# Performance work log

Hardware: AMD Instinct MI355X
Metric: run time of the kernel (lower is better)

## Reference

```python
import jax, jax.numpy as jnp
import numpy as np

B, N, E, DIN, DOUT = 8, 4096, 160, 15, 15


def _mha(q, k, v, in_w, in_b, out_w, out_b, h):
    # torch.nn.MultiheadAttention math: packed in_proj, per-head scaled dot attn, out_proj.
    e = q.shape[-1]
    d = e // h
    scale = 1.0 / np.sqrt(d)

    def proj(x, w, b):
        y = x @ w.T + b
        return jnp.moveaxis(y.reshape(y.shape[:-1] + (h, d)), -2, -3)  # [..., h, L, d]

    qh = proj(q, in_w[:e], in_b[:e])
    kh = proj(k, in_w[e:2 * e], in_b[e:2 * e])
    vh = proj(v, in_w[2 * e:], in_b[2 * e:])
    a = jax.nn.softmax(jnp.einsum('...hld,...hmd->...hlm', qh, kh) * scale, axis=-1)
    o = jnp.einsum('...hlm,...hmd->...hld', a, vh)
    o = jnp.moveaxis(o, -3, -2).reshape(q.shape)
    return o @ out_w.T + out_b


def _attn_layer(seq, Wq, Wk, Wv, in_w, in_b, out_w, out_b, h):
    # AttentionLayer: extra Wq/Wk/Wv projections feeding the MHA
    return _mha(seq @ Wq, seq @ Wk, seq @ Wv, in_w, in_b, out_w, out_b, h)


def setup_inputs():
    key = jax.random.key(0)
    ks = jax.random.split(key, 20)
    s = 1.0 / np.sqrt(E)
    p = lambda i, shape: jax.random.normal(ks[i], shape, dtype=jnp.float32) * s
    return {
        'X_batch': jax.random.normal(ks[0], (B, N, E), dtype=jnp.float32),
        'in_idx': jax.random.randint(ks[1], (B, N, DIN), 0, N),
        'out_idx': jax.random.randint(ks[2], (B, N, DOUT), 0, N),
        'iWq': p(3, (E, E)), 'iWk': p(4, (E, E)), 'iWv': p(5, (E, E)),
        'i_in_w': p(6, (3 * E, E)), 'i_in_b': jnp.zeros(3 * E, jnp.float32),
        'i_out_w': p(7, (E, E)), 'i_out_b': jnp.zeros(E, jnp.float32),
        'oWq': p(8, (E, E)), 'oWk': p(9, (E, E)), 'oWv': p(10, (E, E)),
        'o_in_w': p(11, (3 * E, E)), 'o_in_b': jnp.zeros(3 * E, jnp.float32),
        'o_out_w': p(12, (E, E)), 'o_out_b': jnp.zeros(E, jnp.float32),
        'f_in_w': p(13, (3 * E, E)), 'f_in_b': jnp.zeros(3 * E, jnp.float32),
        'f_out_w': p(14, (E, E)), 'f_out_b': jnp.zeros(E, jnp.float32),
        'lin_w': p(15, (E, E)), 'lin_b': jnp.zeros(E, jnp.float32),
    }


def reference(X_batch, in_idx, out_idx,
              iWq, iWk, iWv, i_in_w, i_in_b, i_out_w, i_out_b,
              oWq, oWk, oWv, o_in_w, o_in_b, o_out_w, o_out_b,
              f_in_w, f_in_b, f_out_w, f_out_b, lin_w, lin_b):
    b_ix = jnp.arange(X_batch.shape[0])[:, None, None]
    self_f = X_batch[:, :, None, :]                                   # [B,N,1,E]
    seq_in = jnp.concatenate([self_f, X_batch[b_ix, in_idx]], axis=2)  # [B,N,1+DIN,E]
    seq_out = jnp.concatenate([self_f, X_batch[b_ix, out_idx]], axis=2)
    a_in = _attn_layer(seq_in, iWq, iWk, iWv, i_in_w, i_in_b, i_out_w, i_out_b, 5)
    a_out = _attn_layer(seq_out, oWq, oWk, oWv, o_in_w, o_in_b, o_out_w, o_out_b, 5)
    a = jnp.concatenate([a_in, a_out], axis=2)                         # [B,N,2+DIN+DOUT,E]
    f = _mha(a, a, a, f_in_w, f_in_b, f_out_w, f_out_b, 1)
    pooled = jnp.max(f, axis=2)                                        # max over sequence dim
    return jax.nn.elu(pooled @ lin_w.T + lin_b)
```

## Files before the change

### kernel.cpp

```cpp
#include <hip/hip_runtime.h>
#include <hip/hip_bf16.h>
#include <math.h>

#define NTH 256

typedef __bf16 bf16x8 __attribute__((ext_vector_type(8)));
typedef float  f32x4  __attribute__((ext_vector_type(4)));
typedef unsigned short ushort;
typedef ushort u16x8 __attribute__((ext_vector_type(8)));

__device__ __forceinline__ ushort f2bf(float x){
    union { float f; unsigned int u; } v; v.f = x;
    unsigned int r = v.u + 0x7fffu + ((v.u >> 16) & 1u);
    return (ushort)(r >> 16);
}
__device__ __forceinline__ float bf2f(ushort h){
    union { unsigned int u; float f; } v; v.u = ((unsigned int)h) << 16;
    return v.f;
}

__global__ void prep_combined_bf(const float* __restrict__ Wq, const float* __restrict__ Wk,
                                 const float* __restrict__ Wv, const float* __restrict__ in_w,
                                 ushort* __restrict__ dh)
{
    int o = blockIdx.x*NTH + threadIdx.x;
    if (o >= 76800) return;
    int c = o/160, j = o - c*160;
    const float* Wsel = (c<160) ? Wq : (c<320) ? Wk : Wv;
    const float* wrow = Wsel + j*160;
    const float* irow = in_w + c*160;
    float s = 0.f;
    for (int k=0;k<160;k++) s = fmaf(wrow[k], irow[k], s);
    dh[o] = f2bf(s);
}

__global__ void prep_H_split(const float* __restrict__ f_in_w, const float* __restrict__ out_w,
                             ushort* __restrict__ dh, float* __restrict__ tmp)
{
    int o = blockIdx.x*NTH + threadIdx.x;
    if (o >= 76800) return;
    int n = o/160, k = o - n*160;
    float s = 0.f;
    for (int c=0;c<160;c++) s = fmaf(f_in_w[n*160+c], out_w[c*160+k], s);
    if (n < 320) dh[o] = f2bf(s);
    else         tmp[(n-320)*160 + k] = s;
}

__global__ void prep_H_fold(const float* __restrict__ fo, const float* __restrict__ Hv,
                            ushort* __restrict__ dh)
{
    int o = blockIdx.x*NTH + threadIdx.x;
    if (o >= 25600) return;
    int n = o/160, k = o - n*160;
    float s = 0.f;
    for (int j=0;j<160;j++) s = fmaf(fo[n*160+j], Hv[j*160+k], s);
    dh[(320+n)*160 + k] = f2bf(s);
}

__global__ void prep_cvec(const float* __restrict__ f_in_w, const float* __restrict__ out_b,
                          const float* __restrict__ f_in_b, float* __restrict__ cvt)
{
    int n = blockIdx.x*NTH + threadIdx.x;
    if (n >= 480) return;
    float s = f_in_b[n];
    for (int c=0;c<160;c++) s = fmaf(f_in_w[n*160+c], out_b[c], s);
    cvt[n] = s;
}

__global__ void prep_cvec_fold(const float* __restrict__ fo, const float* __restrict__ cvt,
                               float* __restrict__ cv)
{
    int n = blockIdx.x*NTH + threadIdx.x;
    if (n >= 480) return;
    if (n < 320){ cv[n] = cvt[n]; return; }
    int m = n - 320;
    float s = 0.f;
    for (int j=0;j<160;j++) s = fmaf(fo[m*160+j], cvt[320+j], s);
    cv[n] = s;
}

__global__ void prep_conv_bf1(const float* __restrict__ src, ushort* __restrict__ dh, int n)
{
    int o = blockIdx.x*NTH + threadIdx.x;
    if (o >= n) return;
    dh[o] = f2bf(src[o]);
}

__global__ void prep_conv_bf2(const float* __restrict__ src,
                              ushort* __restrict__ dh, ushort* __restrict__ dl, int n)
{
    int o = blockIdx.x*NTH + threadIdx.x;
    if (o >= n) return;
    float s = src[o];
    ushort h = f2bf(s);
    dh[o] = h; dl[o] = f2bf(s - bf2f(h));
}

__global__ __launch_bounds__(NTH)
void gemm_mfma_lin(const float* __restrict__ A,
                   const ushort* __restrict__ Wh, const ushort* __restrict__ Wl,
                   const float* __restrict__ bias, float* __restrict__ C, int N)
{
    __shared__ ushort sAh[128*40], sAl[128*40];
    __shared__ ushort sWh[160*40], sWl[160*40];

    const int tid = threadIdx.x;
    const int lane = tid & 63, wave = tid >> 6;
    const int wm = wave >> 1, wn = wave & 1;
    const int ln = lane & 15, g = lane >> 4;
    const long m0 = (long)blockIdx.x * 128;
    const int  n0 = blockIdx.y * 160;

    f32x4 acc[4][5];
#pragma unroll
    for (int mt=0;mt<4;mt++)
#pragma unroll
        for (int nt=0;nt<5;nt++)
#pragma unroll
            for (int r=0;r<4;r++) acc[mt][nt][r] = 0.f;

    for (int k0=0;k0<160;k0+=32){
#pragma unroll
        for (int i=0;i<4;i++){
            int f = tid + 256*i;
            int m = f >> 3, seg = f & 7;
            float4 v = *(const float4*)(A + (m0+m)*160 + k0 + seg*4);
            ushort4 hv, lv;
            hv.x = f2bf(v.x); lv.x = f2bf(v.x - bf2f(hv.x));
            hv.y = f2bf(v.y); lv.y = f2bf(v.y - bf2f(hv.y));
            hv.z = f2bf(v.z); lv.z = f2bf(v.z - bf2f(hv.z));
            hv.w = f2bf(v.w); lv.w = f2bf(v.w - bf2f(hv.w));
            *(ushort4*)(sAh + m*40 + seg*4) = hv;
            *(ushort4*)(sAl + m*40 + seg*4) = lv;
        }
#pragma unroll
        for (int i=0;i<5;i++){
            int e = tid + 256*i;
            int pl = (e >= 640);
            int idx = pl ? e-640 : e;
            int n = idx >> 2, seg = idx & 3;
            const ushort* src = (pl ? Wl : Wh) + (long)(n0+n)*160 + k0 + seg*8;
            ushort* dst = (pl ? sWl : sWh) + n*40 + seg*8;
            *(uint4*)dst = *(const uint4*)src;
        }
        __syncthreads();

        bf16x8 ah[4], al[4];
#pragma unroll
        for (int mt=0;mt<4;mt++){
            int off = (wm*64 + mt*16 + ln)*40 + g*8;
            ah[mt] = *(const bf16x8*)(sAh + off);
            al[mt] = *(const bf16x8*)(sAl + off);
        }
#pragma unroll
        for (int nt=0;nt<5;nt++){
            int offw = (wn*80 + nt*16 + ln)*40 + g*8;
            bf16x8 bh = *(const bf16x8*)(sWh + offw);
            bf16x8 bl = *(const bf16x8*)(sWl + offw);
#pragma unroll
            for (int mt=0;mt<4;mt++){
                acc[mt][nt] = __builtin_amdgcn_mfma_f32_16x16x32_bf16(ah[mt], bh, acc[mt][nt], 0,0,0);
                acc[mt][nt] = __builtin_amdgcn_mfma_f32_16x16x32_bf16(al[mt], bh, acc[mt][nt], 0,0,0);
                acc[mt][nt] = __builtin_amdgcn_mfma_f32_16x16x32_bf16(ah[mt], bl, acc[mt][nt], 0,0,0);
            }
        }
        __syncthreads();
    }

#pragma unroll
    for (int nt=0;nt<5;nt++){
        int col = n0 + wn*80 + nt*16 + ln;
        float bv = bias[col];
#pragma unroll
        for (int mt=0;mt<4;mt++){
#pragma unroll
            for (int r=0;r<4;r++){
                long row = m0 + wm*64 + mt*16 + g*4 + r;
                float x = acc[mt][nt][r] + bv;
                x = x > 0.f ? x : expm1f(x);
                C[row*N + col] = x;
            }
        }
    }
}

__global__ __launch_bounds__(NTH)
void gemm_bf(const ushort* __restrict__ A0, const ushort* __restrict__ A1,
             const ushort* __restrict__ Wh0, const ushort* __restrict__ Wh1,
             const float* __restrict__ b0, const float* __restrict__ b1,
             ushort* __restrict__ C0, ushort* __restrict__ C1, int N)
{
    const int z = blockIdx.z;
    const ushort* A  = z ? A1 : A0;
    const ushort* Wh = z ? Wh1 : Wh0;
    const float* bias = z ? b1 : b0;
    ushort* C = z ? C1 : C0;

    __shared__ ushort sA[128*40];
    __shared__ ushort sW[160*40];

    const int tid = threadIdx.x;
    const int lane = tid & 63, wave = tid >> 6;
    const int wm = wave >> 1, wn = wave & 1;
    const int ln = lane & 15, g = lane >> 4;
    const long m0 = (long)blockIdx.x * 128;
    const int  n0 = blockIdx.y * 160;

    f32x4 acc[4][5];
#pragma unroll
    for (int mt=0;mt<4;mt++)
#pragma unroll
        for (int nt=0;nt<5;nt++)
#pragma unroll
            for (int r=0;r<4;r++) acc[mt][nt][r] = 0.f;

    for (int k0=0;k0<160;k0+=32){
#pragma unroll
        for (int i=0;i<2;i++){
            int e = tid + 256*i;
            int m = e >> 2, seg = e & 3;
            *(uint4*)(sA + m*40 + seg*8) =
                *(const uint4*)(A + (m0+m)*160 + k0 + seg*8);
        }
#pragma unroll
        for (int i=0;i<3;i++){
            int e = tid + 256*i;
            if (e < 640){
                int n = e >> 2, seg = e & 3;
                *(uint4*)(sW + n*40 + seg*8) =
                    *(const uint4*)(Wh + (long)(n0+n)*160 + k0 + seg*8);
            }
        }
        __syncthreads();

        bf16x8 af[4];
#pragma unroll
        for (int mt=0;mt<4;mt++)
            af[mt] = *(const bf16x8*)(sA + (wm*64 + mt*16 + ln)*40 + g*8);
#pragma unroll
        for (int nt=0;nt<5;nt++){
            bf16x8 bh = *(const bf16x8*)(sW + (wn*80 + nt*16 + ln)*40 + g*8);
#pragma unroll
            for (int mt=0;mt<4;mt++)
                acc[mt][nt] = __builtin_amdgcn_mfma_f32_16x16x32_bf16(af[mt], bh, acc[mt][nt], 0,0,0);
        }
        __syncthreads();
    }

#pragma unroll
    for (int nt=0;nt<5;nt++){
        int col = n0 + wn*80 + nt*16 + ln;
        float bv = bias[col];
#pragma unroll
        for (int mt=0;mt<4;mt++){
#pragma unroll
            for (int r=0;r<4;r++){
                long row = m0 + wm*64 + mt*16 + g*4 + r;
                C[row*N + col] = f2bf(acc[mt][nt][r] + bv);
            }
        }
    }
}

#define XST 504
__global__ __launch_bounds__(512)
void mega_node(const ushort* __restrict__ XPi, const ushort* __restrict__ XPo,
               const int* __restrict__ in_idx, const int* __restrict__ out_idx,
               const ushort* __restrict__ Hi, const ushort* __restrict__ Ho,
               const float* __restrict__ c_i, const float* __restrict__ c_o,
               const float* __restrict__ fb, float* __restrict__ pooled)
{
    __shared__ ushort lds[36352];

    const int tid  = threadIdx.x;
    const int lane = tid & 63, w = tid >> 6;
    const int ln = lane & 15, g = lane >> 4;
    const int bid = ((int)blockIdx.x & 7) * 2048 + ((int)blockIdx.x >> 3);
    const int nl0 = bid * 2;

    ushort* XPg = lds;
    ushort* sO  = lds + 16128;
    ushort* sPh = lds + 26880;

    const int ndA = w & 1, p = w >> 1;
    const int nodeA = nl0 + ndA;
    const int bb = nodeA >> 12, nn = nodeA & 4095;
    int idx0 = nn, idx1 = nn;
    if (lane >= 1 && lane < 16){
        idx0 = in_idx [(long)nodeA*15 + lane-1];
        idx1 = out_idx[(long)nodeA*15 + lane-1];
    }

#pragma unroll
    for (int i=0;i<4;i++){
        int e = i*256 + p*64 + lane;
        if (e < 960){
            int r = e/60, c = e - r*60;
            int rowg = __shfl(idx0, r);
            *(uint4*)(XPg + ndA*16*XST + r*XST + c*8) =
                *(const uint4*)(XPi + (long)(bb*4096 + rowg)*480 + c*8);
        }
    }
    __syncthreads();

    const float scale1 = 0.17677669529663687f;
#pragma unroll
    for (int l=0; l<2; l++){
        if (l == 1){
#pragma unroll
            for (int i=0;i<4;i++){
                int e = i*256 + p*64 + lane;
                if (e < 960){
                    int r = e/60, c = e - r*60;
                    int rowg = __shfl(idx1, r);
                    *(uint4*)(XPg + ndA*16*XST + r*XST + c*8) =
                        *(const uint4*)(XPo + (long)(bb*4096 + rowg)*480 + c*8);
                }
            }
            __syncthreads();
        }

#pragma unroll
        for (int rep=0; rep<2; rep++){
            int t = w + rep*8;
            if (t < 10){
                int nd = t/5, h = t - 5*(t/5);
                const ushort* xg = XPg + nd*16*XST;
                bf16x8 ka = *(const bf16x8*)(xg + ln*XST + 160 + h*32 + g*8);
                bf16x8 qb = *(const bf16x8*)(xg + ln*XST +       h*32 + g*8);
                f32x4 s = {0.f,0.f,0.f,0.f};
                s = __builtin_amdgcn_mfma_f32_16x16x32_bf16(ka, qb, s, 0,0,0);
                float x[4], m = -1e30f;
#pragma unroll
                for (int r=0;r<4;r++){ x[r] = s[r]*scale1; m = fmaxf(m, x[r]); }
                m = fmaxf(m, __shfl_xor(m, 16));
                m = fmaxf(m, __shfl_xor(m, 32));
                float e0[4], sum = 0.f;
#pragma unroll
                for (int r=0;r<4;r++){ e0[r] = __expf(x[r]-m); sum += e0[r]; }
                sum += __shfl_xor(sum, 16);
                sum += __shfl_xor(sum, 32);
                float inv = 1.f/sum;
                ushort4 pw;
                pw.x = f2bf(e0[0]*inv); pw.y = f2bf(e0[1]*inv);
                pw.z = f2bf(e0[2]*inv); pw.w = f2bf(e0[3]*inv);
                *(ushort4*)(sPh + t*384 + ln*24 + g*4) = pw;
            }
        }
        __syncthreads();

#pragma unroll
        for (int rep=0; rep<2; rep++){
            int t = w + rep*8;
            if (t < 10){
                int nd = t/5, h = t - 5*(t/5);
                const ushort* xg = XPg + nd*16*XST;
                u16x8 ta;
#pragma unroll
                for (int jj=0;jj<8;jj++) ta[jj] = 0;
                if (g < 2) ta = *(const u16x8*)(sPh + t*384 + ln*24 + g*8);
                bf16x8 ap = *(bf16x8*)&ta;
#pragma unroll
                for (int half=0; half<2; half++){
                    u16x8 tb;
#pragma unroll
                    for (int jj=0;jj<8;jj++) tb[jj] = 0;
                    if (g < 2){
#pragma unroll
                        for (int jj=0;jj<8;jj++)
                            tb[jj] = xg[(g*8+jj)*XST + 320 + h*32 + half*16 + ln];
                    }
                    bf16x8 bv = *(bf16x8*)&tb;
                    f32x4 o = {0.f,0.f,0.f,0.f};
                    o = __builtin_amdgcn_mfma_f32_16x16x32_bf16(ap, bv, o, 0,0,0);
#pragma unroll
                    for (int r=0;r<4;r++)
                        sO[((nd*2+l)*16 + g*4+r)*168 + h*32 + half*16 + ln] = f2bf(o[r]);
                }
            }
        }
        __syncthreads();
    }

    const int wl = w >> 2, wn = w & 3;
    const ushort* Hw = wl ? Ho  : Hi;
    const float*  cw = wl ? c_o : c_i;

    bf16x8 ofr[2][5];
#pragma unroll
    for (int nd=0; nd<2; nd++)
#pragma unroll
        for (int kc=0; kc<5; kc++)
            ofr[nd][kc] = *(const bf16x8*)(sO + ((nd*2+wl)*16 + ln)*168 + kc*32 + g*8);

    bf16x8 hf[5], hn[5];
#pragma unroll
    for (int kc=0; kc<5; kc++)
        hf[kc] = *(const bf16x8*)(Hw + (long)(wn*16 + ln)*160 + kc*32 + g*8);
    __syncthreads();

    ushort* sFQ = lds;
    ushort* sVt = lds + 20992;
    ushort* sPf = lds + 33792;

    for (int t=0; t<8; t++){
        const int cg = t*4 + wn;
        if (t < 7){
            const int cgn = cg + 4;
            if (cgn < 30){
                const ushort* hrow = Hw + (long)(cgn*16 + ln)*160;
#pragma unroll
                for (int kc=0; kc<5; kc++)
                    hn[kc] = *(const bf16x8*)(hrow + kc*32 + g*8);
            }
        }

        if (cg < 30){
            f32x4 acc[2];
#pragma unroll
            for (int nd=0; nd<2; nd++)
#pragma unroll
                for (int r=0;r<4;r++) acc[nd][r] = 0.f;

#pragma unroll
            for (int kc=0; kc<5; kc++)
#pragma unroll
                for (int nd=0; nd<2; nd++)
                    acc[nd] = __builtin_amdgcn_mfma_f32_16x16x32_bf16(hf[kc], ofr[nd][kc], acc[nd], 0,0,0);

            const int cb0 = cg*16 + g*4;
            float4 cb = *(const float4*)(cw + cb0);
            if (cg < 20){
#pragma unroll
                for (int nd=0; nd<2; nd++){
                    ushort4 w4;
                    w4.x = f2bf(acc[nd][0] + cb.x);
                    w4.y = f2bf(acc[nd][1] + cb.y);
                    w4.z = f2bf(acc[nd][2] + cb.z);
                    w4.w = f2bf(acc[nd][3] + cb.w);
                    *(ushort4*)(sFQ + nd*10496 + (wl*16 + ln)*328 + cb0) = w4;
                }
            } else {
                const int c0 = cb0 - 320;
#pragma unroll
                for (int nd=0; nd<2; nd++){
                    sVt[nd*6400 + (c0+0)*40 + wl*16 + ln] = f2bf(acc[nd][0] + cb.x);
                    sVt[nd*6400 + (c0+1)*40 + wl*16 + ln] = f2bf(acc[nd][1] + cb.y);
                    sVt[nd*6400 + (c0+2)*40 + wl*16 + ln] = f2bf(acc[nd][2] + cb.z);
                    sVt[nd*6400 + (c0+3)*40 + wl*16 + ln] = f2bf(acc[nd][3] + cb.w);
                }
            }
        }
#pragma unroll
        for (int kc=0; kc<5; kc++) hf[kc] = hn[kc];
    }
    __syncthreads();

    const int nd = w >> 1, th = w & 1;
    const ushort* myQ = sFQ + nd*10496;
    const ushort* myV = sVt + nd*6400;
    ushort*       myP = sPf + nd*1280;

    if (w < 4){
        f32x4 sc[2];
#pragma unroll
        for (int tj=0; tj<2; tj++){
            f32x4 a = {0.f,0.f,0.f,0.f};
#pragma unroll
            for (int kc=0; kc<5; kc++){
                bf16x8 ka = *(const bf16x8*)(myQ + (tj*16+ln)*328 + 160 + kc*32 + g*8);
                bf16x8 qb = *(const bf16x8*)(myQ + (th*16+ln)*328 +       kc*32 + g*8);
                a = __builtin_amdgcn_mfma_f32_16x16x32_bf16(ka, qb, a, 0,0,0);
            }
            sc[tj] = a;
        }

        const float scale = 0.07905694150420949f;
        float x[2][4], m = -1e30f;
#pragma unroll
        for (int tj=0; tj<2; tj++)
#pragma unroll
            for (int r=0;r<4;r++){ x[tj][r] = sc[tj][r]*scale; m = fmaxf(m, x[tj][r]); }
        m = fmaxf(m, __shfl_xor(m, 16));
        m = fmaxf(m, __shfl_xor(m, 32));
        float sum = 0.f;
#pragma unroll
        for (int tj=0; tj<2; tj++)
#pragma unroll
            for (int r=0;r<4;r++){ x[tj][r] = __expf(x[tj][r]-m); sum += x[tj][r]; }
        sum += __shfl_xor(sum, 16);
        sum += __shfl_xor(sum, 32);
        float inv = 1.f/sum;
#pragma unroll
        for (int tj=0; tj<2; tj++){
            ushort4 pw;
            pw.x = f2bf(x[tj][0]*inv); pw.y = f2bf(x[tj][1]*inv);
            pw.z = f2bf(x[tj][2]*inv); pw.w = f2bf(x[tj][3]*inv);
            *(ushort4*)(myP + (th*16+ln)*40 + tj*16 + g*4) = pw;
        }
    }
    __syncthreads();

    if (w < 4){
        bf16x8 ap[2];
#pragma unroll
        for (int mi=0; mi<2; mi++)
            ap[mi] = *(const bf16x8*)(myP + (mi*16+ln)*40 + g*8);

        const long node = (long)nl0 + nd;
#pragma unroll
        for (int nt5=0; nt5<5; nt5++){
            const int nt = th*5 + nt5;
            bf16x8 bv = *(const bf16x8*)(myV + (nt*16+ln)*40 + g*8);
            float vmax = -1e30f;
#pragma unroll
            for (int mi=0; mi<2; mi++){
                f32x4 o = {0.f,0.f,0.f,0.f};
                o = __builtin_amdgcn_mfma_f32_16x16x32_bf16(ap[mi], bv, o, 0,0,0);
#pragma unroll
                for (int r=0;r<4;r++) vmax = fmaxf(vmax, o[r]);
            }
            vmax = fmaxf(vmax, __shfl_xor(vmax, 16));
            vmax = fmaxf(vmax, __shfl_xor(vmax, 32));
            if (g == 0){
                int col = nt*16 + ln;
                pooled[node*160 + col] = vmax + fb[col];
            }
        }
    }
}

extern "C" void kernel_launch(void* const* d_in, const int* in_sizes, int n_in,
                              void* d_out, int out_size, void* d_ws, size_t ws_size,
                              hipStream_t stream)
{
    const float* X       = (const float*)d_in[0];
    const int*   in_idx  = (const int*)  d_in[1];
    const int*   out_idx = (const int*)  d_in[2];
    const float* iWq     = (const float*)d_in[3];
    const float* iWk     = (const float*)d_in[4];
    const float* iWv     = (const float*)d_in[5];
    const float* i_in_w  = (const float*)d_in[6];
    const float* i_in_b  = (const float*)d_in[7];
    const float* i_out_w = (const float*)d_in[8];
    const float* i_out_b = (const float*)d_in[9];
    const float* oWq     = (const float*)d_in[10];
    const float* oWk     = (const float*)d_in[11];
    const float* oWv     = (const float*)d_in[12];
    const float* o_in_w  = (const float*)d_in[13];
    const float* o_in_b  = (const float*)d_in[14];
    const float* o_out_w = (const float*)d_in[15];
    const float* o_out_b = (const float*)d_in[16];
    const float* f_in_w  = (const float*)d_in[17];
    const float* f_in_b  = (const float*)d_in[18];
    const float* f_out_w = (const float*)d_in[19];
    const float* f_out_b = (const float*)d_in[20];
    const float* lin_w   = (const float*)d_in[21];
    const float* lin_b   = (const float*)d_in[22];

    float* ws = (float*)d_ws;
    float* pooled = ws;
    float* c_i    = pooled + 5242880;
    float* c_o    = c_i + 480;
    float* cvt_i  = c_o + 480;
    float* cvt_o  = cvt_i + 480;
    float* Hvt_i  = cvt_o + 480;
    float* Hvt_o  = Hvt_i + 25600;
    ushort* Xb    = (ushort*)(Hvt_o + 25600);
    ushort* XPb_i = Xb + 5242880;
    ushort* XPb_o = XPb_i + 15728640;
    ushort* Wci_h = XPb_o + 15728640;
    ushort* Wco_h = Wci_h + 76800;
    ushort* Hi_h  = Wco_h + 76800;
    ushort* Ho_h  = Hi_h  + 76800;
    ushort* li_h  = Ho_h  + 76800;
    ushort* li_l  = li_h  + 25600;

    prep_combined_bf<<<300,NTH,0,stream>>>(iWq,iWk,iWv,i_in_w, Wci_h);
    prep_combined_bf<<<300,NTH,0,stream>>>(oWq,oWk,oWv,o_in_w, Wco_h);
    prep_H_split<<<300,NTH,0,stream>>>(f_in_w, i_out_w, Hi_h, Hvt_i);
    prep_H_split<<<300,NTH,0,stream>>>(f_in_w, o_out_w, Ho_h, Hvt_o);
    prep_H_fold<<<100,NTH,0,stream>>>(f_out_w, Hvt_i, Hi_h);
    prep_H_fold<<<100,NTH,0,stream>>>(f_out_w, Hvt_o, Ho_h);
    prep_cvec<<<2,NTH,0,stream>>>(f_in_w, i_out_b, f_in_b, cvt_i);
    prep_cvec<<<2,NTH,0,stream>>>(f_in_w, o_out_b, f_in_b, cvt_o);
    prep_cvec_fold<<<2,NTH,0,stream>>>(f_out_w, cvt_i, c_i);
    prep_cvec_fold<<<2,NTH,0,stream>>>(f_out_w, cvt_o, c_o);
    prep_conv_bf2<<<100,NTH,0,stream>>>(lin_w, li_h, li_l, 25600);
    prep_conv_bf1<<<20480,NTH,0,stream>>>(X, Xb, 5242880);

    dim3 g1(256, 3, 2);
    gemm_bf<<<g1,NTH,0,stream>>>(Xb, Xb, Wci_h, Wco_h, i_in_b, o_in_b,
                                 XPb_i, XPb_o, 480);

    mega_node<<<16384,512,0,stream>>>(XPb_i, XPb_o, in_idx, out_idx,
                                      Hi_h, Ho_h, c_i, c_o, f_out_b, pooled);

    dim3 g6(256, 1);
    gemm_mfma_lin<<<g6,NTH,0,stream>>>(pooled, li_h, li_l, lin_b, (float*)d_out, 160);
}
```

Baseline: 786.3 us.

## Merge per-head softmax and PV passes, add MFMA priority hints, use native bf16 cast

Fuses the per-head score/softmax loop with the following P·V loop, removing one block-wide barrier per iteration. Each wave now reads back the probabilities it just wrote, which only works if the reading lanes map to the writing wave. Wraps the MFMA sections in s_setprio hints, issues the two pooled-output MFMAs back to back, and replaces the manual round-to-nearest float-to-bf16 routine with the compiler's native conversion.

```diff
diff --git a/kernel.cpp b/kernel.cpp
--- a/kernel.cpp
+++ b/kernel.cpp
@@ -10,9 +10,9 @@
 typedef ushort u16x8 __attribute__((ext_vector_type(8)));
 
 __device__ __forceinline__ ushort f2bf(float x){
-    union { float f; unsigned int u; } v; v.f = x;
-    unsigned int r = v.u + 0x7fffu + ((v.u >> 16) & 1u);
-    return (ushort)(r >> 16);
+    union { __bf16 b; ushort u; } v;
+    v.b = (__bf16)x;
+    return v.u;
 }
 __device__ __forceinline__ float bf2f(ushort h){
     union { unsigned int u; float f; } v; v.u = ((unsigned int)h) << 16;
@@ -326,10 +326,13 @@
             if (t < 10){
                 int nd = t/5, h = t - 5*(t/5);
                 const ushort* xg = XPg + nd*16*XST;
+
                 bf16x8 ka = *(const bf16x8*)(xg + ln*XST + 160 + h*32 + g*8);
                 bf16x8 qb = *(const bf16x8*)(xg + ln*XST +       h*32 + g*8);
                 f32x4 s = {0.f,0.f,0.f,0.f};
+                __builtin_amdgcn_s_setprio(1);
                 s = __builtin_amdgcn_mfma_f32_16x16x32_bf16(ka, qb, s, 0,0,0);
+                __builtin_amdgcn_s_setprio(0);
                 float x[4], m = -1e30f;
 #pragma unroll
                 for (int r=0;r<4;r++){ x[r] = s[r]*scale1; m = fmaxf(m, x[r]); }
@@ -345,16 +348,7 @@
                 pw.x = f2bf(e0[0]*inv); pw.y = f2bf(e0[1]*inv);
                 pw.z = f2bf(e0[2]*inv); pw.w = f2bf(e0[3]*inv);
                 *(ushort4*)(sPh + t*384 + ln*24 + g*4) = pw;
-            }
-        }
-        __syncthreads();
-
-#pragma unroll
-        for (int rep=0; rep<2; rep++){
-            int t = w + rep*8;
-            if (t < 10){
-                int nd = t/5, h = t - 5*(t/5);
-                const ushort* xg = XPg + nd*16*XST;
+
                 u16x8 ta;
 #pragma unroll
                 for (int jj=0;jj<8;jj++) ta[jj] = 0;
@@ -372,7 +366,9 @@
                     }
                     bf16x8 bv = *(bf16x8*)&tb;
                     f32x4 o = {0.f,0.f,0.f,0.f};
+                    __builtin_amdgcn_s_setprio(1);
                     o = __builtin_amdgcn_mfma_f32_16x16x32_bf16(ap, bv, o, 0,0,0);
+                    __builtin_amdgcn_s_setprio(0);
 #pragma unroll
                     for (int r=0;r<4;r++)
                         sO[((nd*2+l)*16 + g*4+r)*168 + h*32 + half*16 + ln] = f2bf(o[r]);
@@ -422,11 +418,13 @@
 #pragma unroll
                 for (int r=0;r<4;r++) acc[nd][r] = 0.f;
 
+            __builtin_amdgcn_s_setprio(1);
 #pragma unroll
             for (int kc=0; kc<5; kc++)
 #pragma unroll
                 for (int nd=0; nd<2; nd++)
                     acc[nd] = __builtin_amdgcn_mfma_f32_16x16x32_bf16(hf[kc], ofr[nd][kc], acc[nd], 0,0,0);
+            __builtin_amdgcn_s_setprio(0);
 
             const int cb0 = cg*16 + g*4;
             float4 cb = *(const float4*)(cw + cb0);
@@ -466,12 +464,14 @@
 #pragma unroll
         for (int tj=0; tj<2; tj++){
             f32x4 a = {0.f,0.f,0.f,0.f};
+            __builtin_amdgcn_s_setprio(1);
 #pragma unroll
             for (int kc=0; kc<5; kc++){
                 bf16x8 ka = *(const bf16x8*)(myQ + (tj*16+ln)*328 + 160 + kc*32 + g*8);
                 bf16x8 qb = *(const bf16x8*)(myQ + (th*16+ln)*328 +       kc*32 + g*8);
                 a = __builtin_amdgcn_mfma_f32_16x16x32_bf16(ka, qb, a, 0,0,0);
             }
+            __builtin_amdgcn_s_setprio(0);
             sc[tj] = a;
         }
 
@@ -513,13 +513,13 @@
             const int nt = th*5 + nt5;
             bf16x8 bv = *(const bf16x8*)(myV + (nt*16+ln)*40 + g*8);
             float vmax = -1e30f;
-#pragma unroll
-            for (int mi=0; mi<2; mi++){
-                f32x4 o = {0.f,0.f,0.f,0.f};
-                o = __builtin_amdgcn_mfma_f32_16x16x32_bf16(ap[mi], bv, o, 0,0,0);
-#pragma unroll
-                for (int r=0;r<4;r++) vmax = fmaxf(vmax, o[r]);
-            }
+            __builtin_amdgcn_s_setprio(1);
+            f32x4 o0 = {0.f,0.f,0.f,0.f}, o1 = {0.f,0.f,0.f,0.f};
+            o0 = __builtin_amdgcn_mfma_f32_16x16x32_bf16(ap[0], bv, o0, 0,0,0);
+            o1 = __builtin_amdgcn_mfma_f32_16x16x32_bf16(ap[1], bv, o1, 0,0,0);
+            __builtin_amdgcn_s_setprio(0);
+#pragma unroll
+            for (int r=0;r<4;r++) vmax = fmaxf(vmax, fmaxf(o0[r], o1[r]));
             vmax = fmaxf(vmax, __shfl_xor(vmax, 16));
             vmax = fmaxf(vmax, __shfl_xor(vmax, 32));
             if (g == 0){
```

After: 802.3 us. 1.02x slower.
